# Optimization experiments

Hardware: AMD Instinct MI355X
Metric: run time of the kernel (lower is better)

## Reference

```python
import jax, jax.numpy as jnp
import numpy as np

B, N, F = 16, 1024, 256
HEADS, K, DOUT = 8, 512, 256
TAU = 1.0
EPS = 1e-08


def setup_inputs() -> dict:
    key = jax.random.key(0)
    k1, k2, k3, k4, k5, k6 = jax.random.split(key, 6)
    return {
        'Q': jax.random.normal(k1, (B, N, F), dtype=jnp.float32),
        'keys': jax.random.uniform(k2, (HEADS, K, F), dtype=jnp.float32),
        'conv_w': jax.random.normal(k3, (HEADS,), dtype=jnp.float32),
        'lin_w': jax.random.normal(k4, (DOUT, F), dtype=jnp.float32) * 0.05,
        'lin_b': jax.random.normal(k5, (DOUT,), dtype=jnp.float32) * 0.05,
        'mask': jax.random.randint(k6, (B, N), 0, 2, dtype=jnp.int32),
    }


def kl_reg(C):
    # C: (B, N, K)
    P = C ** 2
    cn = jnp.sum(C, axis=-2, keepdims=True) + EPS          # sum over N
    P = P / cn
    pn = jnp.sum(P, axis=-1, keepdims=True) + EPS          # sum over K
    P = P / pn
    kl = jnp.sum(P * (jnp.log(P + EPS) - jnp.log(C + EPS)))
    return 100.0 * kl


def memconv_fwd(Q, keys, conv_w, lin_w, lin_b, fmask):
    # pairwise L2 distance Q (B,N,F) vs keys (H,K,F) -> C (B,H,N,K)
    q2 = jnp.sum(Q * Q, axis=-1)                            # (B,N)
    k2 = jnp.sum(keys * keys, axis=-1)                      # (H,K)
    qk = jnp.einsum('bnf,hkf->bhnk', Q, keys)               # (B,H,N,K)
    d2 = q2[:, None, :, None] + k2[None, :, None, :] - 2.0 * qk
    C = jnp.sqrt(jnp.maximum(d2, 0.0))
    em = fmask[:, None, :, None]                            # (B,1,N,1) broadcast
    C = C * em
    # student-t kernel (gmn variant)
    C = (1.0 + C ** 2 / TAU) ** (-(0.5 * TAU + 0.5))
    C = C / jnp.sum(C, axis=-1, keepdims=True)
    C = C * em
    # conv1x1 over heads -> (B,N,K)
    C = jnp.einsum('bhnk,h->bnk', C, conv_w)
    C = jax.nn.softmax(C, axis=-1)
    C = C * fmask[:, :, None]
    kl = kl_reg(C)
    V = jnp.einsum('bnk,bnf->bkf', C, Q)                    # (B,K,F)
    out = jax.nn.leaky_relu(jnp.einsum('bkf,of->bko', V, lin_w) + lin_b, 0.01)
    return out, kl


def reference(Q, keys, conv_w, lin_w, lin_b, mask):
    fmask = mask.astype(Q.dtype)
    return memconv_fwd(Q, keys, conv_w, lin_w, lin_b, fmask)
```

## Files before the change

### kernel.cpp

```cpp
#include <hip/hip_runtime.h>
#include <math.h>

#define Bc 16
#define Nc 1024
#define Fc 256
#define Hc 8
#define Kc 512
#define DOUTc 256
#define EPSc 1e-8f

typedef short v8s __attribute__((ext_vector_type(8)));
typedef float v4f __attribute__((ext_vector_type(4)));

__device__ __forceinline__ float waveReduceSum(float v) {
    v += __shfl_xor(v, 32); v += __shfl_xor(v, 16); v += __shfl_xor(v, 8);
    v += __shfl_xor(v, 4);  v += __shfl_xor(v, 2);  v += __shfl_xor(v, 1);
    return v;
}

__device__ __forceinline__ unsigned short f2bf(float f) {
    unsigned int u = __float_as_uint(f);
    u = (u + 0x7fffu + ((u >> 16) & 1u)) >> 16;
    return (unsigned short)u;
}

__device__ __forceinline__ void lds_barrier() {
    __builtin_amdgcn_s_waitcnt(0xC07F);
    __builtin_amdgcn_s_barrier();
}

__global__ __launch_bounds__(256) void prep_all(
    const float* __restrict__ Q, const float* __restrict__ keys,
    const float* __restrict__ lin_w,
    float* __restrict__ k2g, unsigned short* __restrict__ Kp,
    unsigned short* __restrict__ Qbp, unsigned short* __restrict__ Wp,
    float* __restrict__ cn, float* __restrict__ klout) {
    __shared__ unsigned short T2[32][66];
    const int bx = blockIdx.x;
    const int tid = threadIdx.x;
    if (bx < 64) {
        int wv = tid >> 6, l = tid & 63;
#pragma unroll 4
        for (int rr = 0; rr < 16; rr++) {
            int row = bx * 64 + wv * 16 + rr;
            float4 v = *(const float4*)(keys + (size_t)row * Fc + l * 4);
            float s = v.x * v.x + v.y * v.y + v.z * v.z + v.w * v.w;
            s = waveReduceSum(s);
            if (l == 0) k2g[row] = s + 1.0f;
        }
    } else if (bx < 576) {
        int t = (bx - 64) * 256 + tid;
        int lane = t & 63, ci = t >> 6;
        int ct = ci & 7, ks = (ci >> 3) & 7, wv = (ci >> 6) & 3, h = ci >> 8;
        int qd = lane >> 4, li = lane & 15;
        int col = h * 512 + wv * 128 + ct * 16 + li;
        const float* src = keys + (size_t)col * Fc + ks * 32 + qd * 8;
        float4 a = *(const float4*)src;
        float4 b = *(const float4*)(src + 4);
        *(ushort4*)(Kp + (size_t)t * 8) = make_ushort4(f2bf(a.x), f2bf(a.y), f2bf(a.z), f2bf(a.w));
        *(ushort4*)(Kp + (size_t)t * 8 + 4) = make_ushort4(f2bf(b.x), f2bf(b.y), f2bf(b.z), f2bf(b.w));
    } else if (bx < 2624) {
        int i = bx - 576;
        int n0 = (i & 31) * 32, f0 = ((i >> 5) & 3) * 64, bb = i >> 7;
        {
            int n_l = tid >> 3, f_l = (tid & 7) * 8;
            const float* src = Q + ((size_t)(bb * Nc + n0 + n_l)) * Fc + f0 + f_l;
            float4 a = *(const float4*)src;
            float4 b = *(const float4*)(src + 4);
            T2[n_l][f_l + 0] = f2bf(a.x); T2[n_l][f_l + 1] = f2bf(a.y);
            T2[n_l][f_l + 2] = f2bf(a.z); T2[n_l][f_l + 3] = f2bf(a.w);
            T2[n_l][f_l + 4] = f2bf(b.x); T2[n_l][f_l + 5] = f2bf(b.y);
            T2[n_l][f_l + 6] = f2bf(b.z); T2[n_l][f_l + 7] = f2bf(b.w);
        }
        __syncthreads();
        int c = tid >> 6, L = tid & 63;
        int qd = L >> 4, li = L & 15;
        unsigned short o[8];
#pragma unroll
        for (int j = 0; j < 8; j++) o[j] = T2[qd * 8 + j][c * 16 + li];
        size_t idx = ((((size_t)bb * 16 + (f0 >> 4) + c) * 32 + (n0 >> 5)) * 64 + L) * 8;
        *(ushort4*)(Qbp + idx) = make_ushort4(o[0], o[1], o[2], o[3]);
        *(ushort4*)(Qbp + idx + 4) = make_ushort4(o[4], o[5], o[6], o[7]);
    } else if (bx < 2656) {
        int t = (bx - 2624) * 256 + tid;
        int lane = t & 63, ci = t >> 6;
        int ot = ci >> 3, fs = ci & 7;
        int qd = lane >> 4, li = lane & 15;
        const float* src = lin_w + (size_t)(ot * 16 + li) * Fc + fs * 32 + qd * 8;
        float4 a = *(const float4*)src;
        float4 b = *(const float4*)(src + 4);
        *(ushort4*)(Wp + (size_t)t * 8) = make_ushort4(f2bf(a.x), f2bf(a.y), f2bf(a.z), f2bf(a.w));
        *(ushort4*)(Wp + (size_t)t * 8 + 4) = make_ushort4(f2bf(b.x), f2bf(b.y), f2bf(b.z), f2bf(b.w));
    } else {
        int i = (bx - 2656) * 256 + tid;
        float4 z = make_float4(0.f, 0.f, 0.f, 0.f);
        float4* d = (float4*)(cn + (size_t)i * 16);
        d[0] = z; d[1] = z; d[2] = z; d[3] = z;
        if (bx == 2656 && tid == 0) *klout = 0.f;
    }
}

__global__ __launch_bounds__(512, 2) void cmfma_kernel(
    const float* __restrict__ Q, const unsigned short* __restrict__ Kp,
    const float* __restrict__ k2g, const float* __restrict__ conv_w,
    const int* __restrict__ mask, float* __restrict__ C,
    float* __restrict__ cn, unsigned short* __restrict__ Ctp) {
    __shared__ __align__(16) char uni[36864];
    __shared__ float q2h[8][16];
    __shared__ float msh[64];
    __shared__ float redb[Hc][8][64];
    __shared__ float mslot[8][64];
    __shared__ float eslot[8][64];
    short* Ash = (short*)uni;
    short (*Tb)[36] = (short (*)[36])uni;

    const int tid = threadIdx.x;
    const int wv = tid >> 6, L = tid & 63;
    const int qd = L >> 4, li = L & 15;
    const int gr0 = blockIdx.x * 64;
    const int b = gr0 >> 10;

    {
        int s_ = wv >> 1;
        int ksbase = (wv & 1) * 4;
        const float* qrow = Q + (size_t)(gr0 + s_ * 16 + li) * Fc + qd * 8;
        float q2part = 0.f;
#pragma unroll
        for (int j = 0; j < 4; j++) {
            int ks = ksbase + j;
            float4 a = *(const float4*)(qrow + ks * 32);
            float4 bq = *(const float4*)(qrow + ks * 32 + 4);
            v8s f;
            f[0] = (short)f2bf(a.x);  f[1] = (short)f2bf(a.y);
            f[2] = (short)f2bf(a.z);  f[3] = (short)f2bf(a.w);
            f[4] = (short)f2bf(bq.x); f[5] = (short)f2bf(bq.y);
            f[6] = (short)f2bf(bq.z); f[7] = (short)f2bf(bq.w);
            *(v8s*)&Ash[(((s_ * 8 + ks) * 64) + L) * 8] = f;
            q2part += a.x * a.x + a.y * a.y + a.z * a.z + a.w * a.w +
                      bq.x * bq.x + bq.y * bq.y + bq.z * bq.z + bq.w * bq.w;
        }
        q2part += __shfl_xor(q2part, 16);
        q2part += __shfl_xor(q2part, 32);
        if (qd == 0) q2h[wv][li] = q2part;
    }
    if (tid < 64) msh[tid] = (float)mask[gr0 + tid];

    v4f D[4][4], S[4][4];
#pragma unroll
    for (int s = 0; s < 4; s++)
#pragma unroll
        for (int ct = 0; ct < 4; ct++) {
            D[s][ct] = (v4f){0.f, 0.f, 0.f, 0.f};
            S[s][ct] = (v4f){0.f, 0.f, 0.f, 0.f};
        }

    const unsigned short* kwbase = Kp + (size_t)L * 8;
    v8s Bb[4][4];

#define BLOAD(slot, hn)                                                            \
    do {                                                                           \
        const unsigned short* pb =                                                 \
            kwbase + (size_t)((((hn) >> 3) & 7) * 256 + (wv >> 1) * 64 +           \
                              ((hn) & 7) * 8 + (wv & 1) * 4) * 512;                \
        Bb[slot][0] = *(const v8s*)(pb);                                           \
        Bb[slot][1] = *(const v8s*)(pb + 512);                                     \
        Bb[slot][2] = *(const v8s*)(pb + 1024);                                    \
        Bb[slot][3] = *(const v8s*)(pb + 1536);                                    \
    } while (0)

#define LDA(dst, kk2)                                                              \
    do {                                                                           \
        _Pragma("unroll") for (int s = 0; s < 4; s++)                              \
            dst[s] = *(const v8s*)&Ash[((s * 8 + (kk2)) * 64 + L) * 8];            \
    } while (0)

    BLOAD(0, 0);
    BLOAD(1, 1);
    lds_barrier();
    v8s Aa[4], Ab[4];
    LDA(Aa, 0);

#define KSTEP(kk, ACUR, ANXT)                                                      \
    do {                                                                           \
        BLOAD((kk + 2) & 3, h * 8 + kk + 2);                                       \
        LDA(ANXT, ((kk) + 1) & 7);                                                 \
        __builtin_amdgcn_s_setprio(1);                                             \
        _Pragma("unroll") for (int s = 0; s < 4; s++)                              \
            _Pragma("unroll") for (int ct = 0; ct < 4; ct++)                       \
                D[s][ct] = __builtin_amdgcn_mfma_f32_16x16x32_bf16(                \
                    ACUR[s], Bb[(kk) & 3][ct], D[s][ct], 0, 0, 0);                 \
        __builtin_amdgcn_s_setprio(0);                                             \
        ;                                                                          \
    } while (0)

    for (int h = 0; h < Hc; ++h) {
        KSTEP(0, Aa, Ab);
        float k2r[4];
#pragma unroll
        for (int ct = 0; ct < 4; ct++)
            k2r[ct] = k2g[h * Kc + wv * 64 + ct * 16 + li];
        KSTEP(1, Ab, Aa); KSTEP(2, Aa, Ab); KSTEP(3, Ab, Aa);
        KSTEP(4, Aa, Ab); KSTEP(5, Ab, Aa); KSTEP(6, Aa, Ab); KSTEP(7, Ab, Aa);

        float rs[4][4];
        v4f q2v[4];
#pragma unroll
        for (int s = 0; s < 4; s++) {
            q2v[s] = *(const v4f*)&q2h[2 * s][qd * 4];
            v4f t2 = *(const v4f*)&q2h[2 * s + 1][qd * 4];
            q2v[s] += t2;
#pragma unroll
            for (int r = 0; r < 4; r++) rs[s][r] = 0.f;
        }
#pragma unroll
        for (int ct = 0; ct < 4; ct++) {
            float k2v = k2r[ct];
#pragma unroll
            for (int s = 0; s < 4; s++)
#pragma unroll
                for (int r = 0; r < 4; r++) {
                    float x = fmaf(-2.f, D[s][ct][r], q2v[s][r] + k2v);
                    float t = __builtin_amdgcn_rcpf(fmaxf(x, 1.0f));
                    D[s][ct][r] = t;
                    rs[s][r] += t;
                }
        }
#pragma unroll
        for (int s = 0; s < 4; s++)
#pragma unroll
            for (int r = 0; r < 4; r++) {
                rs[s][r] += __shfl_xor(rs[s][r], 1, 16);
                rs[s][r] += __shfl_xor(rs[s][r], 2, 16);
                rs[s][r] += __shfl_xor(rs[s][r], 4, 16);
                rs[s][r] += __shfl_xor(rs[s][r], 8, 16);
            }
        if (li == 0) {
#pragma unroll
            for (int s = 0; s < 4; s++)
#pragma unroll
                for (int r = 0; r < 4; r++)
                    redb[h][wv][s * 16 + qd * 4 + r] = rs[s][r];
        }
        lds_barrier();
        float wh = conv_w[h];
#pragma unroll
        for (int s = 0; s < 4; s++) {
            v4f tot = *(const v4f*)&redb[h][0][s * 16 + qd * 4];
#pragma unroll
            for (int w = 1; w < 8; w++) tot += *(const v4f*)&redb[h][w][s * 16 + qd * 4];
#pragma unroll
            for (int r = 0; r < 4; r++) {
                float sc = wh * __builtin_amdgcn_rcpf(tot[r]);
#pragma unroll
                for (int ct = 0; ct < 4; ct++) {
                    S[s][ct][r] += sc * D[s][ct][r];
                    D[s][ct][r] = 0.f;
                }
            }
        }
    }
#undef KSTEP
#undef LDA
#undef BLOAD

    float mx[4][4];
#pragma unroll
    for (int s = 0; s < 4; s++)
#pragma unroll
        for (int r = 0; r < 4; r++) {
            float m = S[s][0][r];
            m = fmaxf(m, S[s][1][r]); m = fmaxf(m, S[s][2][r]); m = fmaxf(m, S[s][3][r]);
            m = fmaxf(m, __shfl_xor(m, 1, 16));
            m = fmaxf(m, __shfl_xor(m, 2, 16));
            m = fmaxf(m, __shfl_xor(m, 4, 16));
            m = fmaxf(m, __shfl_xor(m, 8, 16));
            mx[s][r] = m;
        }
    if (li == 0) {
#pragma unroll
        for (int s = 0; s < 4; s++)
#pragma unroll
            for (int r = 0; r < 4; r++) mslot[wv][s * 16 + qd * 4 + r] = mx[s][r];
    }
    lds_barrier();
#pragma unroll
    for (int s = 0; s < 4; s++) {
        v4f m = *(const v4f*)&mslot[0][s * 16 + qd * 4];
#pragma unroll
        for (int w = 1; w < 8; w++) {
            v4f t = *(const v4f*)&mslot[w][s * 16 + qd * 4];
#pragma unroll
            for (int r = 0; r < 4; r++) m[r] = fmaxf(m[r], t[r]);
        }
#pragma unroll
        for (int r = 0; r < 4; r++) mx[s][r] = m[r];
    }
    float es[4][4];
#pragma unroll
    for (int s = 0; s < 4; s++)
#pragma unroll
        for (int r = 0; r < 4; r++) {
            float e0 = __expf(S[s][0][r] - mx[s][r]);
            float e1 = __expf(S[s][1][r] - mx[s][r]);
            float e2 = __expf(S[s][2][r] - mx[s][r]);
            float e3 = __expf(S[s][3][r] - mx[s][r]);
            S[s][0][r] = e0; S[s][1][r] = e1; S[s][2][r] = e2; S[s][3][r] = e3;
            float e = e0 + e1 + e2 + e3;
            e += __shfl_xor(e, 1, 16);
            e += __shfl_xor(e, 2, 16);
            e += __shfl_xor(e, 4, 16);
            e += __shfl_xor(e, 8, 16);
            es[s][r] = e;
        }
    if (li == 0) {
#pragma unroll
        for (int s = 0; s < 4; s++)
#pragma unroll
            for (int r = 0; r < 4; r++) eslot[wv][s * 16 + qd * 4 + r] = es[s][r];
    }
    lds_barrier();
    float inv[4][4];
#pragma unroll
    for (int s = 0; s < 4; s++) {
        v4f tot = *(const v4f*)&eslot[0][s * 16 + qd * 4];
#pragma unroll
        for (int w = 1; w < 8; w++) tot += *(const v4f*)&eslot[w][s * 16 + qd * 4];
        v4f mr = *(const v4f*)&msh[s * 16 + qd * 4];
#pragma unroll
        for (int r = 0; r < 4; r++) inv[s][r] = mr[r] / tot[r];
    }

    const int ns0 = (gr0 & 1023) >> 5;
    float colsum[4] = {0.f, 0.f, 0.f, 0.f};
#pragma unroll
    for (int p = 0; p < 2; p++) {
        if (p == 1) lds_barrier();
#pragma unroll
        for (int ct = 0; ct < 4; ct++) {
            int k = wv * 64 + ct * 16 + li;
#pragma unroll
            for (int s2 = 0; s2 < 2; s2++) {
                int s = p * 2 + s2;
                float cv[4];
#pragma unroll
                for (int r = 0; r < 4; r++) {
                    cv[r] = S[s][ct][r] * inv[s][r];
                    C[(size_t)(gr0 + s * 16 + qd * 4 + r) * Kc + k] = cv[r];
                    colsum[ct] += cv[r];
                }
                short4 t4;
                t4.x = (short)f2bf(cv[0]); t4.y = (short)f2bf(cv[1]);
                t4.z = (short)f2bf(cv[2]); t4.w = (short)f2bf(cv[3]);
                *(short4*)&Tb[k][s2 * 16 + qd * 4] = t4;
            }
        }
        lds_barrier();
        {
            int kt = tid >> 4, klo = tid & 15;
            size_t cbase = (((size_t)b * 32 + kt) * 32 + ns0 + p) * 512;
#pragma unroll
            for (int q2i = 0; q2i < 4; q2i++) {
                short4 lo = *(short4*)&Tb[tid][q2i * 8];
                short4 hi = *(short4*)&Tb[tid][q2i * 8 + 4];
                short4* d = (short4*)(Ctp + cbase + (size_t)(q2i * 16 + klo) * 8);
                d[0] = lo; d[1] = hi;
            }
        }
    }
#pragma unroll
    for (int ct = 0; ct < 4; ct++) {
        int k = wv * 64 + ct * 16 + li;
        float cs = colsum[ct];
        cs += __shfl_xor(cs, 16);
        cs += __shfl_xor(cs, 32);
        if (qd == 0) atomicAdd(&cn[b * Kc + k], cs);
    }
}

__global__ __launch_bounds__(256) void klv_kernel(
    const unsigned short* __restrict__ Ctp, const unsigned short* __restrict__ Qbp,
    unsigned short* __restrict__ Vp, const float* __restrict__ C,
    const float* __restrict__ cn, float* __restrict__ klout) {
    __shared__ short Vt[64][76];
    __shared__ float red[4];
    int tid = threadIdx.x;
    int bx = blockIdx.x;
    if (bx < 512) {
        int w = tid >> 6, L = tid & 63;
        int qd = L >> 4, li = L & 15;
        int wr = w >> 1, wc = w & 1;
        int bb = bx >> 5;
        int rem = bx & 31;
        int ktb = rem >> 2, ftb = rem & 3;
        int KT0 = ktb * 4 + wr * 2;
        int FT0 = ftb * 4 + wc * 2;
        const unsigned short* pa0 = Ctp + (((size_t)bb * 32 + KT0) * 32) * 512 + L * 8;
        const unsigned short* pa1 = pa0 + (size_t)32 * 512;
        const unsigned short* pb0 = Qbp + (((size_t)bb * 16 + FT0) * 32) * 512 + L * 8;
        const unsigned short* pb1 = pb0 + (size_t)32 * 512;
        v4f acc[2][2];
#pragma unroll
        for (int a = 0; a < 2; a++)
#pragma unroll
            for (int c = 0; c < 2; c++) acc[a][c] = (v4f){0.f, 0.f, 0.f, 0.f};

        v8s Ae0 = *(const v8s*)pa0, Ae1 = *(const v8s*)pa1;
        v8s Be0 = *(const v8s*)pb0, Be1 = *(const v8s*)pb1;
        v8s Ao0 = *(const v8s*)(pa0 + 512), Ao1 = *(const v8s*)(pa1 + 512);
        v8s Bo0 = *(const v8s*)(pb0 + 512), Bo1 = *(const v8s*)(pb1 + 512);
        for (int ns = 0; ns < 32; ns += 2) {
            int n2 = (ns + 2) & 31;
            int n3 = (ns + 3) & 31;
            acc[0][0] = __builtin_amdgcn_mfma_f32_16x16x32_bf16(Ae0, Be0, acc[0][0], 0, 0, 0);
            acc[0][1] = __builtin_amdgcn_mfma_f32_16x16x32_bf16(Ae0, Be1, acc[0][1], 0, 0, 0);
            acc[1][0] = __builtin_amdgcn_mfma_f32_16x16x32_bf16(Ae1, Be0, acc[1][0], 0, 0, 0);
            acc[1][1] = __builtin_amdgcn_mfma_f32_16x16x32_bf16(Ae1, Be1, acc[1][1], 0, 0, 0);
            Ae0 = *(const v8s*)(pa0 + n2 * 512); Ae1 = *(const v8s*)(pa1 + n2 * 512);
            Be0 = *(const v8s*)(pb0 + n2 * 512); Be1 = *(const v8s*)(pb1 + n2 * 512);
            acc[0][0] = __builtin_amdgcn_mfma_f32_16x16x32_bf16(Ao0, Bo0, acc[0][0], 0, 0, 0);
            acc[0][1] = __builtin_amdgcn_mfma_f32_16x16x32_bf16(Ao0, Bo1, acc[0][1], 0, 0, 0);
            acc[1][0] = __builtin_amdgcn_mfma_f32_16x16x32_bf16(Ao1, Bo0, acc[1][0], 0, 0, 0);
            acc[1][1] = __builtin_amdgcn_mfma_f32_16x16x32_bf16(Ao1, Bo1, acc[1][1], 0, 0, 0);
            Ao0 = *(const v8s*)(pa0 + n3 * 512); Ao1 = *(const v8s*)(pa1 + n3 * 512);
            Bo0 = *(const v8s*)(pb0 + n3 * 512); Bo1 = *(const v8s*)(pb1 + n3 * 512);
        }
#pragma unroll
        for (int a = 0; a < 2; a++)
#pragma unroll
            for (int c = 0; c < 2; c++)
#pragma unroll
                for (int r = 0; r < 4; r++)
                    Vt[(wr * 2 + a) * 16 + qd * 4 + r][(wc * 2 + c) * 16 + li] =
                        (short)f2bf(acc[a][c][r]);
        __syncthreads();
        {
            int ci = tid >> 5, s5 = tid & 31;
            int mtl = ci >> 1, fsl = ci & 1;
            size_t mt_g = (size_t)bb * 32 + ktb * 4 + mtl;
            size_t fs_g = (size_t)ftb * 2 + fsl;
#pragma unroll
            for (int half = 0; half < 2; half++) {
                int L2 = s5 + half * 32;
                int qd2 = L2 >> 4, li2 = L2 & 15;
                short4 x0 = *(short4*)&Vt[mtl * 16 + li2][fsl * 32 + qd2 * 8];
                short4 x1 = *(short4*)&Vt[mtl * 16 + li2][fsl * 32 + qd2 * 8 + 4];
                short4* d = (short4*)(Vp + ((mt_g * 8 + fs_g) * 64 + L2) * 8);
                d[0] = x0; d[1] = x1;
            }
        }
    } else {
        int bk = bx - 512;
        int w = tid >> 6, l = tid & 63;
        int b0 = (bk * 16) >> 10;
        const float* np = cn + b0 * Kc + l * 8;
        v4f n0 = *(const v4f*)np;
        v4f n1 = *(const v4f*)(np + 4);
        float rn[8];
#pragma unroll
        for (int j = 0; j < 4; j++) {
            rn[j] = __builtin_amdgcn_rcpf(n0[j] + EPSc);
            rn[4 + j] = __builtin_amdgcn_rcpf(n1[j] + EPSc);
        }
        float kacc = 0.f;
#pragma unroll
        for (int rr = 0; rr < 4; rr++) {
            int row = bk * 16 + w * 4 + rr;
            const float* cp = C + (size_t)row * Kc + l * 8;
            v4f c0 = *(const v4f*)cp;
            v4f c1 = *(const v4f*)(cp + 4);
            float cc[8] = {c0[0], c0[1], c0[2], c0[3], c1[0], c1[1], c1[2], c1[3]};
            float p[8];
#pragma unroll
            for (int j = 0; j < 8; j++) p[j] = cc[j] * cc[j] * rn[j];
            float s = p[0] + p[1] + p[2] + p[3] + p[4] + p[5] + p[6] + p[7];
            float pn = waveReduceSum(s) + EPSc;
            float rpn = __builtin_amdgcn_rcpf(pn);
#pragma unroll
            for (int j = 0; j < 8; j++) {
                float P = p[j] * rpn;
                kacc += P * __logf((P + EPSc) * __builtin_amdgcn_rcpf(cc[j] + EPSc));
            }
        }
        kacc = waveReduceSum(kacc);
        if (l == 0) red[w] = kacc;
        __syncthreads();
        if (tid == 0)
            atomicAdd(klout, 100.f * (red[0] + red[1] + red[2] + red[3]));
    }
}

__global__ __launch_bounds__(256) void ofma_kernel(
    const unsigned short* __restrict__ Vp, const unsigned short* __restrict__ Wp,
    const float* __restrict__ bias, float* __restrict__ out) {
    int tid = threadIdx.x;
    int w = tid >> 6, L = tid & 63;
    int qd = L >> 4, li = L & 15;
    int wr = w >> 1, wc = w & 1;
    int MT0 = blockIdx.x * 4 + wr * 2;
    int OT0 = blockIdx.y * 4 + wc * 2;
    const unsigned short* pa0 = Vp + ((size_t)MT0 * 8) * 512 + L * 8;
    const unsigned short* pa1 = pa0 + (size_t)8 * 512;
    const unsigned short* pb0 = Wp + ((size_t)OT0 * 8) * 512 + L * 8;
    const unsigned short* pb1 = pb0 + (size_t)8 * 512;
    v4f acc[2][2];
#pragma unroll
    for (int a = 0; a < 2; a++)
#pragma unroll
        for (int c = 0; c < 2; c++) acc[a][c] = (v4f){0.f, 0.f, 0.f, 0.f};
    v8s Ae0 = *(const v8s*)pa0, Ae1 = *(const v8s*)pa1;
    v8s Be0 = *(const v8s*)pb0, Be1 = *(const v8s*)pb1;
    v8s Ao0 = *(const v8s*)(pa0 + 512), Ao1 = *(const v8s*)(pa1 + 512);
    v8s Bo0 = *(const v8s*)(pb0 + 512), Bo1 = *(const v8s*)(pb1 + 512);
#pragma unroll
    for (int fs = 0; fs < 8; fs += 2) {
        int n2 = (fs + 2) & 7;
        int n3 = (fs + 3) & 7;
        acc[0][0] = __builtin_amdgcn_mfma_f32_16x16x32_bf16(Ae0, Be0, acc[0][0], 0, 0, 0);
        acc[0][1] = __builtin_amdgcn_mfma_f32_16x16x32_bf16(Ae0, Be1, acc[0][1], 0, 0, 0);
        acc[1][0] = __builtin_amdgcn_mfma_f32_16x16x32_bf16(Ae1, Be0, acc[1][0], 0, 0, 0);
        acc[1][1] = __builtin_amdgcn_mfma_f32_16x16x32_bf16(Ae1, Be1, acc[1][1], 0, 0, 0);
        Ae0 = *(const v8s*)(pa0 + n2 * 512); Ae1 = *(const v8s*)(pa1 + n2 * 512);
        Be0 = *(const v8s*)(pb0 + n2 * 512); Be1 = *(const v8s*)(pb1 + n2 * 512);
        acc[0][0] = __builtin_amdgcn_mfma_f32_16x16x32_bf16(Ao0, Bo0, acc[0][0], 0, 0, 0);
        acc[0][1] = __builtin_amdgcn_mfma_f32_16x16x32_bf16(Ao0, Bo1, acc[0][1], 0, 0, 0);
        acc[1][0] = __builtin_amdgcn_mfma_f32_16x16x32_bf16(Ao1, Bo0, acc[1][0], 0, 0, 0);
        acc[1][1] = __builtin_amdgcn_mfma_f32_16x16x32_bf16(Ao1, Bo1, acc[1][1], 0, 0, 0);
        Ao0 = *(const v8s*)(pa0 + n3 * 512); Ao1 = *(const v8s*)(pa1 + n3 * 512);
        Bo0 = *(const v8s*)(pb0 + n3 * 512); Bo1 = *(const v8s*)(pb1 + n3 * 512);
    }
#pragma unroll
    for (int c = 0; c < 2; c++) {
        float bv = bias[(OT0 + c) * 16 + li];
#pragma unroll
        for (int a = 0; a < 2; a++)
#pragma unroll
            for (int r = 0; r < 4; r++) {
                int m = (MT0 + a) * 16 + qd * 4 + r;
                int o = (OT0 + c) * 16 + li;
                float x = acc[a][c][r] + bv;
                out[(size_t)m * DOUTc + o] = x > 0.f ? x : 0.01f * x;
            }
    }
}

extern "C" void kernel_launch(void* const* d_in, const int* in_sizes, int n_in,
                              void* d_out, int out_size, void* d_ws, size_t ws_size,
                              hipStream_t stream) {
    const float* Q = (const float*)d_in[0];
    const float* keys = (const float*)d_in[1];
    const float* conv_w = (const float*)d_in[2];
    const float* lin_w = (const float*)d_in[3];
    const float* lin_b = (const float*)d_in[4];
    const int* mask = (const int*)d_in[5];

    float* out = (float*)d_out;
    float* kl = out + (size_t)Bc * Kc * DOUTc;

    float* ws = (float*)d_ws;
    float* C = ws;
    float* k2 = C + (size_t)Bc * Nc * Kc;
    float* cn = k2 + (size_t)Hc * Kc;
    unsigned short* Kp = (unsigned short*)(cn + (size_t)Bc * Kc);
    unsigned short* Ctp = Kp + (size_t)Hc * Kc * Fc;
    unsigned short* Qbp = Ctp + (size_t)Bc * Nc * Kc;
    unsigned short* Vp = Qbp + (size_t)Bc * Nc * Fc;
    unsigned short* Wp = Vp + (size_t)Bc * Kc * Fc;

    prep_all<<<2658, 256, 0, stream>>>(Q, keys, lin_w, k2, Kp, Qbp, Wp, cn, kl);
    cmfma_kernel<<<Bc * Nc / 64, 512, 0, stream>>>(Q, Kp, k2, conv_w, mask, C, cn, Ctp);
    klv_kernel<<<1536, 256, 0, stream>>>(Ctp, Qbp, Vp, C, cn, kl);
    ofma_kernel<<<dim3(Bc * Kc / 64, DOUTc / 64), 256, 0, stream>>>(Vp, Wp, lin_b, out);
}
```

Baseline: 175.6 us.

## Enlarge V-GEMM tiles in klv kernel and zero-init accumulators via first MFMA

The V = C^T Q GEMM part of klv_kernel now uses 128x128 output tiles per block, with each wave computing 4x4 MFMA tiles instead of 2x2. This cuts the V blocks from 512 to 128 and raises operand reuse from global loads. In cmfma the first k-step of each head passes a zero accumulator directly instead of clearing D explicitly, and the ofma loads are simplified to plain per-step loads. The larger tiles raise register and LDS pressure and leave fewer blocks for the V work, which may reduce overlap with the KL blocks.

Measured after the change: 174.0 us. Within noise of the previous version (-0.9%).

```diff
diff --git a/kernel.cpp b/kernel.cpp
--- a/kernel.cpp
+++ b/kernel.cpp
@@ -149,10 +149,8 @@
 #pragma unroll
     for (int s = 0; s < 4; s++)
 #pragma unroll
-        for (int ct = 0; ct < 4; ct++) {
-            D[s][ct] = (v4f){0.f, 0.f, 0.f, 0.f};
+        for (int ct = 0; ct < 4; ct++)
             S[s][ct] = (v4f){0.f, 0.f, 0.f, 0.f};
-        }
 
     const unsigned short* kwbase = Kp + (size_t)L * 8;
     v8s Bb[4][4];
@@ -180,6 +178,18 @@
     v8s Aa[4], Ab[4];
     LDA(Aa, 0);
 
+#define KSTEP0(ACUR, ANXT)                                                         \
+    do {                                                                           \
+        BLOAD(2, h * 8 + 2);                                                       \
+        LDA(ANXT, 1);                                                              \
+        __builtin_amdgcn_s_setprio(1);                                             \
+        _Pragma("unroll") for (int s = 0; s < 4; s++)                              \
+            _Pragma("unroll") for (int ct = 0; ct < 4; ct++)                       \
+                D[s][ct] = __builtin_amdgcn_mfma_f32_16x16x32_bf16(                \
+                    ACUR[s], Bb[0][ct], (v4f){0.f, 0.f, 0.f, 0.f}, 0, 0, 0);       \
+        __builtin_amdgcn_s_setprio(0);                                             \
+    } while (0)
+
 #define KSTEP(kk, ACUR, ANXT)                                                      \
     do {                                                                           \
         BLOAD((kk + 2) & 3, h * 8 + kk + 2);                                       \
@@ -190,11 +200,10 @@
                 D[s][ct] = __builtin_amdgcn_mfma_f32_16x16x32_bf16(                \
                     ACUR[s], Bb[(kk) & 3][ct], D[s][ct], 0, 0, 0);                 \
         __builtin_amdgcn_s_setprio(0);                                             \
-        ;                                                                          \
     } while (0)
 
     for (int h = 0; h < Hc; ++h) {
-        KSTEP(0, Aa, Ab);
+        KSTEP0(Aa, Ab);
         float k2r[4];
 #pragma unroll
         for (int ct = 0; ct < 4; ct++)
@@ -252,14 +261,13 @@
             for (int r = 0; r < 4; r++) {
                 float sc = wh * __builtin_amdgcn_rcpf(tot[r]);
 #pragma unroll
-                for (int ct = 0; ct < 4; ct++) {
+                for (int ct = 0; ct < 4; ct++)
                     S[s][ct][r] += sc * D[s][ct][r];
-                    D[s][ct][r] = 0.f;
-                }
             }
         }
     }
 #undef KSTEP
+#undef KSTEP0
 #undef LDA
 #undef BLOAD
 
@@ -381,75 +389,83 @@
     const unsigned short* __restrict__ Ctp, const unsigned short* __restrict__ Qbp,
     unsigned short* __restrict__ Vp, const float* __restrict__ C,
     const float* __restrict__ cn, float* __restrict__ klout) {
-    __shared__ short Vt[64][76];
+    __shared__ short Vt[128][132];
     __shared__ float red[4];
     int tid = threadIdx.x;
     int bx = blockIdx.x;
-    if (bx < 512) {
+    if (bx < 128) {
         int w = tid >> 6, L = tid & 63;
         int qd = L >> 4, li = L & 15;
         int wr = w >> 1, wc = w & 1;
-        int bb = bx >> 5;
-        int rem = bx & 31;
-        int ktb = rem >> 2, ftb = rem & 3;
-        int KT0 = ktb * 4 + wr * 2;
-        int FT0 = ftb * 4 + wc * 2;
-        const unsigned short* pa0 = Ctp + (((size_t)bb * 32 + KT0) * 32) * 512 + L * 8;
-        const unsigned short* pa1 = pa0 + (size_t)32 * 512;
-        const unsigned short* pb0 = Qbp + (((size_t)bb * 16 + FT0) * 32) * 512 + L * 8;
-        const unsigned short* pb1 = pb0 + (size_t)32 * 512;
-        v4f acc[2][2];
-#pragma unroll
-        for (int a = 0; a < 2; a++)
-#pragma unroll
-            for (int c = 0; c < 2; c++) acc[a][c] = (v4f){0.f, 0.f, 0.f, 0.f};
-
-        v8s Ae0 = *(const v8s*)pa0, Ae1 = *(const v8s*)pa1;
-        v8s Be0 = *(const v8s*)pb0, Be1 = *(const v8s*)pb1;
-        v8s Ao0 = *(const v8s*)(pa0 + 512), Ao1 = *(const v8s*)(pa1 + 512);
-        v8s Bo0 = *(const v8s*)(pb0 + 512), Bo1 = *(const v8s*)(pb1 + 512);
-        for (int ns = 0; ns < 32; ns += 2) {
-            int n2 = (ns + 2) & 31;
-            int n3 = (ns + 3) & 31;
-            acc[0][0] = __builtin_amdgcn_mfma_f32_16x16x32_bf16(Ae0, Be0, acc[0][0], 0, 0, 0);
-            acc[0][1] = __builtin_amdgcn_mfma_f32_16x16x32_bf16(Ae0, Be1, acc[0][1], 0, 0, 0);
-            acc[1][0] = __builtin_amdgcn_mfma_f32_16x16x32_bf16(Ae1, Be0, acc[1][0], 0, 0, 0);
-            acc[1][1] = __builtin_amdgcn_mfma_f32_16x16x32_bf16(Ae1, Be1, acc[1][1], 0, 0, 0);
-            Ae0 = *(const v8s*)(pa0 + n2 * 512); Ae1 = *(const v8s*)(pa1 + n2 * 512);
-            Be0 = *(const v8s*)(pb0 + n2 * 512); Be1 = *(const v8s*)(pb1 + n2 * 512);
-            acc[0][0] = __builtin_amdgcn_mfma_f32_16x16x32_bf16(Ao0, Bo0, acc[0][0], 0, 0, 0);
-            acc[0][1] = __builtin_amdgcn_mfma_f32_16x16x32_bf16(Ao0, Bo1, acc[0][1], 0, 0, 0);
-            acc[1][0] = __builtin_amdgcn_mfma_f32_16x16x32_bf16(Ao1, Bo0, acc[1][0], 0, 0, 0);
-            acc[1][1] = __builtin_amdgcn_mfma_f32_16x16x32_bf16(Ao1, Bo1, acc[1][1], 0, 0, 0);
-            Ao0 = *(const v8s*)(pa0 + n3 * 512); Ao1 = *(const v8s*)(pa1 + n3 * 512);
-            Bo0 = *(const v8s*)(pb0 + n3 * 512); Bo1 = *(const v8s*)(pb1 + n3 * 512);
-        }
-#pragma unroll
-        for (int a = 0; a < 2; a++)
-#pragma unroll
-            for (int c = 0; c < 2; c++)
+        int bb = bx >> 3;
+        int rem = bx & 7;
+        int ktb = rem >> 1, ftb = rem & 1;
+        int KT0 = ktb * 8 + wr * 4;
+        int FT0 = ftb * 8 + wc * 4;
+        const unsigned short* pa[4];
+        const unsigned short* pb[4];
+#pragma unroll
+        for (int a = 0; a < 4; a++)
+            pa[a] = Ctp + (((size_t)bb * 32 + KT0 + a) * 32) * 512 + L * 8;
+#pragma unroll
+        for (int c = 0; c < 4; c++)
+            pb[c] = Qbp + (((size_t)bb * 16 + FT0 + c) * 32) * 512 + L * 8;
+        v4f acc[4][4];
+#pragma unroll
+        for (int a = 0; a < 4; a++)
+#pragma unroll
+            for (int c = 0; c < 4; c++) acc[a][c] = (v4f){0.f, 0.f, 0.f, 0.f};
+
+        v8s A[4], B[4], An[4], Bn[4];
+#pragma unroll
+        for (int a = 0; a < 4; a++) A[a] = *(const v8s*)pa[a];
+#pragma unroll
+        for (int c = 0; c < 4; c++) B[c] = *(const v8s*)pb[c];
+        for (int ns = 0; ns < 32; ns++) {
+            int nn = (ns + 1) & 31;
+#pragma unroll
+            for (int a = 0; a < 4; a++) An[a] = *(const v8s*)(pa[a] + nn * 512);
+#pragma unroll
+            for (int c = 0; c < 4; c++) Bn[c] = *(const v8s*)(pb[c] + nn * 512);
+#pragma unroll
+            for (int a = 0; a < 4; a++)
+#pragma unroll
+                for (int c = 0; c < 4; c++)
+                    acc[a][c] = __builtin_amdgcn_mfma_f32_16x16x32_bf16(
+                        A[a], B[c], acc[a][c], 0, 0, 0);
+#pragma unroll
+            for (int a = 0; a < 4; a++) A[a] = An[a];
+#pragma unroll
+            for (int c = 0; c < 4; c++) B[c] = Bn[c];
+        }
+#pragma unroll
+        for (int a = 0; a < 4; a++)
+#pragma unroll
+            for (int c = 0; c < 4; c++)
 #pragma unroll
                 for (int r = 0; r < 4; r++)
-                    Vt[(wr * 2 + a) * 16 + qd * 4 + r][(wc * 2 + c) * 16 + li] =
+                    Vt[(wr * 4 + a) * 16 + qd * 4 + r][(wc * 4 + c) * 16 + li] =
                         (short)f2bf(acc[a][c][r]);
         __syncthreads();
         {
-            int ci = tid >> 5, s5 = tid & 31;
-            int mtl = ci >> 1, fsl = ci & 1;
-            size_t mt_g = (size_t)bb * 32 + ktb * 4 + mtl;
-            size_t fs_g = (size_t)ftb * 2 + fsl;
-#pragma unroll
-            for (int half = 0; half < 2; half++) {
-                int L2 = s5 + half * 32;
-                int qd2 = L2 >> 4, li2 = L2 & 15;
-                short4 x0 = *(short4*)&Vt[mtl * 16 + li2][fsl * 32 + qd2 * 8];
-                short4 x1 = *(short4*)&Vt[mtl * 16 + li2][fsl * 32 + qd2 * 8 + 4];
-                short4* d = (short4*)(Vp + ((mt_g * 8 + fs_g) * 64 + L2) * 8);
-                d[0] = x0; d[1] = x1;
+            int mtl = tid >> 5, s5 = tid & 31;
+            size_t mt_g = (size_t)bb * 32 + ktb * 8 + mtl;
+#pragma unroll
+            for (int fsl = 0; fsl < 4; fsl++) {
+                size_t fs_g = (size_t)ftb * 4 + fsl;
+#pragma unroll
+                for (int half = 0; half < 2; half++) {
+                    int L2 = s5 + half * 32;
+                    int qd2 = L2 >> 4, li2 = L2 & 15;
+                    short4 x0 = *(short4*)&Vt[mtl * 16 + li2][fsl * 32 + qd2 * 8];
+                    short4 x1 = *(short4*)&Vt[mtl * 16 + li2][fsl * 32 + qd2 * 8 + 4];
+                    short4* d = (short4*)(Vp + ((mt_g * 8 + fs_g) * 64 + L2) * 8);
+                    d[0] = x0; d[1] = x1;
+                }
             }
         }
     } else {
-        int bk = bx - 512;
+        int bk = bx - 128;
         int w = tid >> 6, l = tid & 63;
         int b0 = (bk * 16) >> 10;
         const float* np = cn + b0 * Kc + l * 8;
@@ -507,26 +523,16 @@
     for (int a = 0; a < 2; a++)
 #pragma unroll
         for (int c = 0; c < 2; c++) acc[a][c] = (v4f){0.f, 0.f, 0.f, 0.f};
-    v8s Ae0 = *(const v8s*)pa0, Ae1 = *(const v8s*)pa1;
-    v8s Be0 = *(const v8s*)pb0, Be1 = *(const v8s*)pb1;
-    v8s Ao0 = *(const v8s*)(pa0 + 512), Ao1 = *(const v8s*)(pa1 + 512);
-    v8s Bo0 = *(const v8s*)(pb0 + 512), Bo1 = *(const v8s*)(pb1 + 512);
-#pragma unroll
-    for (int fs = 0; fs < 8; fs += 2) {
-        int n2 = (fs + 2) & 7;
-        int n3 = (fs + 3) & 7;
-        acc[0][0] = __builtin_amdgcn_mfma_f32_16x16x32_bf16(Ae0, Be0, acc[0][0], 0, 0, 0);
-        acc[0][1] = __builtin_amdgcn_mfma_f32_16x16x32_bf16(Ae0, Be1, acc[0][1], 0, 0, 0);
-        acc[1][0] = __builtin_amdgcn_mfma_f32_16x16x32_bf16(Ae1, Be0, acc[1][0], 0, 0, 0);
-        acc[1][1] = __builtin_amdgcn_mfma_f32_16x16x32_bf16(Ae1, Be1, acc[1][1], 0, 0, 0);
-        Ae0 = *(const v8s*)(pa0 + n2 * 512); Ae1 = *(const v8s*)(pa1 + n2 * 512);
-        Be0 = *(const v8s*)(pb0 + n2 * 512); Be1 = *(const v8s*)(pb1 + n2 * 512);
-        acc[0][0] = __builtin_amdgcn_mfma_f32_16x16x32_bf16(Ao0, Bo0, acc[0][0], 0, 0, 0);
-        acc[0][1] = __builtin_amdgcn_mfma_f32_16x16x32_bf16(Ao0, Bo1, acc[0][1], 0, 0, 0);
-        acc[1][0] = __builtin_amdgcn_mfma_f32_16x16x32_bf16(Ao1, Bo0, acc[1][0], 0, 0, 0);
-        acc[1][1] = __builtin_amdgcn_mfma_f32_16x16x32_bf16(Ao1, Bo1, acc[1][1], 0, 0, 0);
-        Ao0 = *(const v8s*)(pa0 + n3 * 512); Ao1 = *(const v8s*)(pa1 + n3 * 512);
-        Bo0 = *(const v8s*)(pb0 + n3 * 512); Bo1 = *(const v8s*)(pb1 + n3 * 512);
+#pragma unroll
+    for (int fs = 0; fs < 8; fs++) {
+        v8s A0 = *(const v8s*)(pa0 + fs * 512);
+        v8s A1 = *(const v8s*)(pa1 + fs * 512);
+        v8s B0 = *(const v8s*)(pb0 + fs * 512);
+        v8s B1 = *(const v8s*)(pb1 + fs * 512);
+        acc[0][0] = __builtin_amdgcn_mfma_f32_16x16x32_bf16(A0, B0, acc[0][0], 0, 0, 0);
+        acc[0][1] = __builtin_amdgcn_mfma_f32_16x16x32_bf16(A0, B1, acc[0][1], 0, 0, 0);
+        acc[1][0] = __builtin_amdgcn_mfma_f32_16x16x32_bf16(A1, B0, acc[1][0], 0, 0, 0);
+        acc[1][1] = __builtin_amdgcn_mfma_f32_16x16x32_bf16(A1, B1, acc[1][1], 0, 0, 0);
     }
 #pragma unroll
     for (int c = 0; c < 2; c++) {
@@ -568,6 +574,6 @@
 
     prep_all<<<2658, 256, 0, stream>>>(Q, keys, lin_w, k2, Kp, Qbp, Wp, cn, kl);
     cmfma_kernel<<<Bc * Nc / 64, 512, 0, stream>>>(Q, Kp, k2, conv_w, mask, C, cn, Ctp);
-    klv_kernel<<<1536, 256, 0, stream>>>(Ctp, Qbp, Vp, C, cn, kl);
+    klv_kernel<<<128 + 1024, 256, 0, stream>>>(Ctp, Qbp, Vp, C, cn, kl);
     ofma_kernel<<<dim3(Bc * Kc / 64, DOUTc / 64), 256, 0, stream>>>(Vp, Wp, lin_b, out);
 }
```

## Fuse Q bf16 transpose-pack into distance kernel and simplify MFMA prefetch loops

Applied to the files above, without the earlier changes.

Packing Q into the transposed bf16 layout moves out of the prep kernel and into cmfma_kernel, which rebuilds it from the bf16 Q tile already in shared memory. This removes 2048 prep blocks and a second full read of Q from global memory. The klv and ofma MFMA loops also replace two-stage even/odd register prefetching with a simpler one-step prefetch or direct loads. In exchange, cmfma gains extra shared-memory reads and global stores, and the simpler loops may hide less load latency.

Result: no change. 172.4 us (-1.8%).

```diff
diff --git a/kernel.cpp b/kernel.cpp
--- a/kernel.cpp
+++ b/kernel.cpp
@@ -30,12 +30,10 @@
 }
 
 __global__ __launch_bounds__(256) void prep_all(
-    const float* __restrict__ Q, const float* __restrict__ keys,
-    const float* __restrict__ lin_w,
+    const float* __restrict__ keys, const float* __restrict__ lin_w,
     float* __restrict__ k2g, unsigned short* __restrict__ Kp,
-    unsigned short* __restrict__ Qbp, unsigned short* __restrict__ Wp,
+    unsigned short* __restrict__ Wp,
     float* __restrict__ cn, float* __restrict__ klout) {
-    __shared__ unsigned short T2[32][66];
     const int bx = blockIdx.x;
     const int tid = threadIdx.x;
     if (bx < 64) {
@@ -59,30 +57,8 @@
         float4 b = *(const float4*)(src + 4);
         *(ushort4*)(Kp + (size_t)t * 8) = make_ushort4(f2bf(a.x), f2bf(a.y), f2bf(a.z), f2bf(a.w));
         *(ushort4*)(Kp + (size_t)t * 8 + 4) = make_ushort4(f2bf(b.x), f2bf(b.y), f2bf(b.z), f2bf(b.w));
-    } else if (bx < 2624) {
-        int i = bx - 576;
-        int n0 = (i & 31) * 32, f0 = ((i >> 5) & 3) * 64, bb = i >> 7;
-        {
-            int n_l = tid >> 3, f_l = (tid & 7) * 8;
-            const float* src = Q + ((size_t)(bb * Nc + n0 + n_l)) * Fc + f0 + f_l;
-            float4 a = *(const float4*)src;
-            float4 b = *(const float4*)(src + 4);
-            T2[n_l][f_l + 0] = f2bf(a.x); T2[n_l][f_l + 1] = f2bf(a.y);
-            T2[n_l][f_l + 2] = f2bf(a.z); T2[n_l][f_l + 3] = f2bf(a.w);
-            T2[n_l][f_l + 4] = f2bf(b.x); T2[n_l][f_l + 5] = f2bf(b.y);
-            T2[n_l][f_l + 6] = f2bf(b.z); T2[n_l][f_l + 7] = f2bf(b.w);
-        }
-        __syncthreads();
-        int c = tid >> 6, L = tid & 63;
-        int qd = L >> 4, li = L & 15;
-        unsigned short o[8];
-#pragma unroll
-        for (int j = 0; j < 8; j++) o[j] = T2[qd * 8 + j][c * 16 + li];
-        size_t idx = ((((size_t)bb * 16 + (f0 >> 4) + c) * 32 + (n0 >> 5)) * 64 + L) * 8;
-        *(ushort4*)(Qbp + idx) = make_ushort4(o[0], o[1], o[2], o[3]);
-        *(ushort4*)(Qbp + idx + 4) = make_ushort4(o[4], o[5], o[6], o[7]);
-    } else if (bx < 2656) {
-        int t = (bx - 2624) * 256 + tid;
+    } else if (bx < 608) {
+        int t = (bx - 576) * 256 + tid;
         int lane = t & 63, ci = t >> 6;
         int ot = ci >> 3, fs = ci & 7;
         int qd = lane >> 4, li = lane & 15;
@@ -92,11 +68,11 @@
         *(ushort4*)(Wp + (size_t)t * 8) = make_ushort4(f2bf(a.x), f2bf(a.y), f2bf(a.z), f2bf(a.w));
         *(ushort4*)(Wp + (size_t)t * 8 + 4) = make_ushort4(f2bf(b.x), f2bf(b.y), f2bf(b.z), f2bf(b.w));
     } else {
-        int i = (bx - 2656) * 256 + tid;
+        int i = (bx - 608) * 256 + tid;
         float4 z = make_float4(0.f, 0.f, 0.f, 0.f);
         float4* d = (float4*)(cn + (size_t)i * 16);
         d[0] = z; d[1] = z; d[2] = z; d[3] = z;
-        if (bx == 2656 && tid == 0) *klout = 0.f;
+        if (bx == 608 && tid == 0) *klout = 0.f;
     }
 }
 
@@ -104,7 +80,8 @@
     const float* __restrict__ Q, const unsigned short* __restrict__ Kp,
     const float* __restrict__ k2g, const float* __restrict__ conv_w,
     const int* __restrict__ mask, float* __restrict__ C,
-    float* __restrict__ cn, unsigned short* __restrict__ Ctp) {
+    float* __restrict__ cn, unsigned short* __restrict__ Ctp,
+    unsigned short* __restrict__ Qbp) {
     __shared__ __align__(16) char uni[36864];
     __shared__ float q2h[8][16];
     __shared__ float msh[64];
@@ -190,7 +167,6 @@
                 D[s][ct] = __builtin_amdgcn_mfma_f32_16x16x32_bf16(                \
                     ACUR[s], Bb[(kk) & 3][ct], D[s][ct], 0, 0, 0);                 \
         __builtin_amdgcn_s_setprio(0);                                             \
-        ;                                                                          \
     } while (0)
 
     for (int h = 0; h < Hc; ++h) {
@@ -262,6 +238,29 @@
 #undef KSTEP
 #undef LDA
 #undef BLOAD
+
+    {
+        int fi = tid >> 4;
+        int nsl = fi >> 4, ft = fi & 15;
+        int sub = tid & 15;
+        size_t qb = (((size_t)b * 16 + ft) * 32 + ((gr0 & 1023) >> 5) + nsl) * 64;
+        const unsigned short* ash = (const unsigned short*)Ash;
+#pragma unroll
+        for (int l4 = 0; l4 < 4; l4++) {
+            int L2 = sub * 4 + l4;
+            int qd2 = L2 >> 4, li2 = L2 & 15;
+            int c = ft * 16 + li2;
+            int cbase = ((c >> 5) * 64 + ((c >> 3) & 3) * 16) * 8 + (c & 7);
+            unsigned short o[8];
+#pragma unroll
+            for (int j = 0; j < 8; j++) {
+                int r = nsl * 32 + qd2 * 8 + j;
+                o[j] = ash[((r >> 4) * 8) * 512 + cbase + (r & 15) * 8];
+            }
+            *(ushort4*)(Qbp + (qb + L2) * 8) = make_ushort4(o[0], o[1], o[2], o[3]);
+            *(ushort4*)(Qbp + (qb + L2) * 8 + 4) = make_ushort4(o[4], o[5], o[6], o[7]);
+        }
+    }
 
     float mx[4][4];
 #pragma unroll
@@ -404,25 +403,19 @@
 #pragma unroll
             for (int c = 0; c < 2; c++) acc[a][c] = (v4f){0.f, 0.f, 0.f, 0.f};
 
-        v8s Ae0 = *(const v8s*)pa0, Ae1 = *(const v8s*)pa1;
-        v8s Be0 = *(const v8s*)pb0, Be1 = *(const v8s*)pb1;
-        v8s Ao0 = *(const v8s*)(pa0 + 512), Ao1 = *(const v8s*)(pa1 + 512);
-        v8s Bo0 = *(const v8s*)(pb0 + 512), Bo1 = *(const v8s*)(pb1 + 512);
-        for (int ns = 0; ns < 32; ns += 2) {
-            int n2 = (ns + 2) & 31;
-            int n3 = (ns + 3) & 31;
-            acc[0][0] = __builtin_amdgcn_mfma_f32_16x16x32_bf16(Ae0, Be0, acc[0][0], 0, 0, 0);
-            acc[0][1] = __builtin_amdgcn_mfma_f32_16x16x32_bf16(Ae0, Be1, acc[0][1], 0, 0, 0);
-            acc[1][0] = __builtin_amdgcn_mfma_f32_16x16x32_bf16(Ae1, Be0, acc[1][0], 0, 0, 0);
-            acc[1][1] = __builtin_amdgcn_mfma_f32_16x16x32_bf16(Ae1, Be1, acc[1][1], 0, 0, 0);
-            Ae0 = *(const v8s*)(pa0 + n2 * 512); Ae1 = *(const v8s*)(pa1 + n2 * 512);
-            Be0 = *(const v8s*)(pb0 + n2 * 512); Be1 = *(const v8s*)(pb1 + n2 * 512);
-            acc[0][0] = __builtin_amdgcn_mfma_f32_16x16x32_bf16(Ao0, Bo0, acc[0][0], 0, 0, 0);
-            acc[0][1] = __builtin_amdgcn_mfma_f32_16x16x32_bf16(Ao0, Bo1, acc[0][1], 0, 0, 0);
-            acc[1][0] = __builtin_amdgcn_mfma_f32_16x16x32_bf16(Ao1, Bo0, acc[1][0], 0, 0, 0);
-            acc[1][1] = __builtin_amdgcn_mfma_f32_16x16x32_bf16(Ao1, Bo1, acc[1][1], 0, 0, 0);
-            Ao0 = *(const v8s*)(pa0 + n3 * 512); Ao1 = *(const v8s*)(pa1 + n3 * 512);
-            Bo0 = *(const v8s*)(pb0 + n3 * 512); Bo1 = *(const v8s*)(pb1 + n3 * 512);
+        v8s A0 = *(const v8s*)pa0, A1 = *(const v8s*)pa1;
+        v8s B0 = *(const v8s*)pb0, B1 = *(const v8s*)pb1;
+        for (int ns = 0; ns < 32; ns++) {
+            int nsn = (ns + 1) & 31;
+            v8s A0n = *(const v8s*)(pa0 + nsn * 512);
+            v8s A1n = *(const v8s*)(pa1 + nsn * 512);
+            v8s B0n = *(const v8s*)(pb0 + nsn * 512);
+            v8s B1n = *(const v8s*)(pb1 + nsn * 512);
+            acc[0][0] = __builtin_amdgcn_mfma_f32_16x16x32_bf16(A0, B0, acc[0][0], 0, 0, 0);
+            acc[0][1] = __builtin_amdgcn_mfma_f32_16x16x32_bf16(A0, B1, acc[0][1], 0, 0, 0);
+            acc[1][0] = __builtin_amdgcn_mfma_f32_16x16x32_bf16(A1, B0, acc[1][0], 0, 0, 0);
+            acc[1][1] = __builtin_amdgcn_mfma_f32_16x16x32_bf16(A1, B1, acc[1][1], 0, 0, 0);
+            A0 = A0n; A1 = A1n; B0 = B0n; B1 = B1n;
         }
 #pragma unroll
         for (int a = 0; a < 2; a++)
@@ -507,26 +500,16 @@
     for (int a = 0; a < 2; a++)
 #pragma unroll
         for (int c = 0; c < 2; c++) acc[a][c] = (v4f){0.f, 0.f, 0.f, 0.f};
-    v8s Ae0 = *(const v8s*)pa0, Ae1 = *(const v8s*)pa1;
-    v8s Be0 = *(const v8s*)pb0, Be1 = *(const v8s*)pb1;
-    v8s Ao0 = *(const v8s*)(pa0 + 512), Ao1 = *(const v8s*)(pa1 + 512);
-    v8s Bo0 = *(const v8s*)(pb0 + 512), Bo1 = *(const v8s*)(pb1 + 512);
-#pragma unroll
-    for (int fs = 0; fs < 8; fs += 2) {
-        int n2 = (fs + 2) & 7;
-        int n3 = (fs + 3) & 7;
-        acc[0][0] = __builtin_amdgcn_mfma_f32_16x16x32_bf16(Ae0, Be0, acc[0][0], 0, 0, 0);
-        acc[0][1] = __builtin_amdgcn_mfma_f32_16x16x32_bf16(Ae0, Be1, acc[0][1], 0, 0, 0);
-        acc[1][0] = __builtin_amdgcn_mfma_f32_16x16x32_bf16(Ae1, Be0, acc[1][0], 0, 0, 0);
-        acc[1][1] = __builtin_amdgcn_mfma_f32_16x16x32_bf16(Ae1, Be1, acc[1][1], 0, 0, 0);
-        Ae0 = *(const v8s*)(pa0 + n2 * 512); Ae1 = *(const v8s*)(pa1 + n2 * 512);
-        Be0 = *(const v8s*)(pb0 + n2 * 512); Be1 = *(const v8s*)(pb1 + n2 * 512);
-        acc[0][0] = __builtin_amdgcn_mfma_f32_16x16x32_bf16(Ao0, Bo0, acc[0][0], 0, 0, 0);
-        acc[0][1] = __builtin_amdgcn_mfma_f32_16x16x32_bf16(Ao0, Bo1, acc[0][1], 0, 0, 0);
-        acc[1][0] = __builtin_amdgcn_mfma_f32_16x16x32_bf16(Ao1, Bo0, acc[1][0], 0, 0, 0);
-        acc[1][1] = __builtin_amdgcn_mfma_f32_16x16x32_bf16(Ao1, Bo1, acc[1][1], 0, 0, 0);
-        Ao0 = *(const v8s*)(pa0 + n3 * 512); Ao1 = *(const v8s*)(pa1 + n3 * 512);
-        Bo0 = *(const v8s*)(pb0 + n3 * 512); Bo1 = *(const v8s*)(pb1 + n3 * 512);
+#pragma unroll
+    for (int fs = 0; fs < 8; fs++) {
+        v8s A0 = *(const v8s*)(pa0 + fs * 512);
+        v8s A1 = *(const v8s*)(pa1 + fs * 512);
+        v8s B0 = *(const v8s*)(pb0 + fs * 512);
+        v8s B1 = *(const v8s*)(pb1 + fs * 512);
+        acc[0][0] = __builtin_amdgcn_mfma_f32_16x16x32_bf16(A0, B0, acc[0][0], 0, 0, 0);
+        acc[0][1] = __builtin_amdgcn_mfma_f32_16x16x32_bf16(A0, B1, acc[0][1], 0, 0, 0);
+        acc[1][0] = __builtin_amdgcn_mfma_f32_16x16x32_bf16(A1, B0, acc[1][0], 0, 0, 0);
+        acc[1][1] = __builtin_amdgcn_mfma_f32_16x16x32_bf16(A1, B1, acc[1][1], 0, 0, 0);
     }
 #pragma unroll
     for (int c = 0; c < 2; c++) {
@@ -566,8 +549,8 @@
     unsigned short* Vp = Qbp + (size_t)Bc * Nc * Fc;
     unsigned short* Wp = Vp + (size_t)Bc * Kc * Fc;
 
-    prep_all<<<2658, 256, 0, stream>>>(Q, keys, lin_w, k2, Kp, Qbp, Wp, cn, kl);
-    cmfma_kernel<<<Bc * Nc / 64, 512, 0, stream>>>(Q, Kp, k2, conv_w, mask, C, cn, Ctp);
+    prep_all<<<610, 256, 0, stream>>>(keys, lin_w, k2, Kp, Wp, cn, kl);
+    cmfma_kernel<<<Bc * Nc / 64, 512, 0, stream>>>(Q, Kp, k2, conv_w, mask, C, cn, Ctp, Qbp);
     klv_kernel<<<1536, 256, 0, stream>>>(Ctp, Qbp, Vp, C, cn, kl);
     ofma_kernel<<<dim3(Bc * Kc / 64, DOUTc / 64), 256, 0, stream>>>(Vp, Wp, lin_b, out);
 }
```
